# Performance work log

Measured on AMD Instinct MI355X. Metric: run time of the kernel, lower is better.

## Reference

```python
import jax, jax.numpy as jnp
import numpy as np

B, N, C_IN, C_EMB, G = 16, 1024, 16, 64, 128
NEG = -1e12


def _lap(m):
    # m @ D^-1/2, transpose, @ D^-1/2  (matches torch code incl. transpose)
    d = jnp.sum(m, axis=1) ** -0.5
    return (m * d[None, :]).T * d[None, :]


def setup_inputs():
    key = jax.random.key(0)
    ks = jax.random.split(key, 16)
    f = jax.random.normal
    return {
        'x': f(ks[0], (B, C_IN, N), jnp.float32),
        'ct': f(ks[1], (B, C_EMB, N), jnp.float32),
        'graph_data': jax.random.uniform(ks[2], (2, N, N), dtype=jnp.float32),
        'emb_w': f(ks[3], (C_EMB, C_IN)) / np.sqrt(C_IN).astype(np.float32),
        'emb_b': f(ks[4], (C_EMB,)) * 0.01,
        'emb2_w': f(ks[5], (N, N)) / np.sqrt(N).astype(np.float32),
        'emb2_b': f(ks[6], (N,)) * 0.01,
        'att_W': f(ks[7], (C_EMB, C_EMB)) / np.sqrt(C_EMB).astype(np.float32),
        'att_a': f(ks[8], (2 * C_EMB, 1)) / np.sqrt(2 * C_EMB).astype(np.float32),
        'att_GL': f(ks[9], (N, G)) / np.sqrt(G).astype(np.float32),
        'uai_w': f(ks[10], (C_EMB, C_EMB)) / np.sqrt(C_EMB).astype(np.float32),
        'uai_b': f(ks[11], (C_EMB,)) * 0.01,
        'lin1_w': f(ks[12], (C_EMB, C_EMB)) / np.sqrt(C_EMB).astype(np.float32),
        'lin2_w': f(ks[13], (C_EMB, C_EMB)) / np.sqrt(C_EMB).astype(np.float32),
        'lin2_b': f(ks[14], (C_EMB,)) * 0.01,
        'ln_w': jnp.ones((C_EMB, N), jnp.float32),
        'ln_b': jnp.zeros((C_EMB, N), jnp.float32),
    }


def reference(x, ct, graph_data, emb_w, emb_b, emb2_w, emb2_b, att_W, att_a,
              att_GL, uai_w, uai_b, lin1_w, lin2_w, lin2_b, ln_w, ln_b):
    # emb: Conv1d k=1 -> leaky_relu -> Linear over node axis N
    h0 = jax.nn.leaky_relu(jnp.einsum('bcn,ec->ben', x, emb_w) + emb_b[None, :, None])
    h0 = jnp.einsum('ben,mn->bem', h0, emb2_w) + emb2_b[None, None, :]
    inp = jnp.swapaxes(h0, 1, 2)  # [B,N,C']

    # InterpositionAttention (repeat/cat factorized: e_ij = leakyrelu(a1.h_i + a2.h_j))
    eye = jnp.eye(N, dtype=x.dtype)
    adj_att = jax.nn.softmax(jax.nn.relu(att_GL @ att_GL.T), axis=-1) + eye
    h = inp @ att_W  # [B,N,C']
    e = jax.nn.leaky_relu((h @ att_a[:C_EMB]) + jnp.swapaxes(h @ att_a[C_EMB:], 1, 2))  # [B,N,N]
    att = jax.nn.softmax(jnp.where(adj_att > 0, e, NEG), axis=2)
    x_att = jnp.swapaxes(jax.nn.relu(att @ h), 1, 2)  # [B,C',N]

    # UAI module (eval mode: dropout off -> all MC samples equal -> sigma = 0)
    mu = jnp.swapaxes(x_att, 1, 2) @ uai_w.T + uai_b  # [B,N,C']
    x_uai = jnp.swapaxes(mu, 1, 2)  # [B,C',N]

    g1 = _lap(graph_data[0] + eye)
    g2 = _lap(graph_data[1] + eye)

    # learned adjacency from pairwise squared distances (cdist p=2, squared)
    xf = jnp.swapaxes(x_uai, 1, 2)  # [B,N,C']
    sq = jnp.sum(xf * xf, axis=-1)
    d2 = jnp.maximum(sq[:, :, None] + sq[:, None, :] - 2.0 * (xf @ jnp.swapaxes(xf, 1, 2)), 0.0)
    gl = jax.nn.softmax(jnp.exp(-d2 / (2.0 * C_EMB)) + eye, axis=-1)  # sigma^2 = emb_size

    def ln(z):  # LayerNorm over last two dims [C', N]
        m = jnp.mean(z, axis=(1, 2), keepdims=True)
        v = jnp.var(z, axis=(1, 2), keepdims=True)
        return (z - m) / jnp.sqrt(v + 1e-5) * ln_w + ln_b

    l1 = lambda z: jnp.einsum('oc,bcn->bon', lin1_w, z)
    l2 = lambda z: jnp.einsum('oc,bcn->bon', lin2_w, z) + lin2_b[None, :, None]

    x_new = ln(l1(x_uai) @ gl + l1(l1(x_uai) @ g1) @ g2)
    ft = jax.nn.gelu(ln(l2(x_uai) @ gl + l2(l2(x_uai) @ g1) @ g2), approximate=False)
    rt = ft  # rt is computed by the identical expression (dropout off)

    ct_new = ft * ct + x_new - ft * x_new
    ht = rt * jax.nn.elu(ct_new) + x_uai - rt * x_uai
    return (ht, ct_new)
```

## Files before the change

kernel.cpp:

```cpp
#include <hip/hip_runtime.h>
#include <math.h>

typedef unsigned short u16;
typedef __attribute__((ext_vector_type(8))) short short8;
typedef __attribute__((ext_vector_type(4))) float floatx4;

constexpr int BATCH = 16;
constexpr int NI = 1024;
constexpr int CE = 64;
constexpr int CI = 16;
constexpr long long NN2  = (long long)NI * NI;
constexpr long long BCN  = (long long)BATCH * CE * NI;
constexpr long long BNv  = (long long)BATCH * NI;
constexpr long long BNN  = (long long)BATCH * NI * NI;
constexpr long long S1 = (long long)CE * NI;
constexpr long long S2 = 2 * S1;
constexpr int ZERON = (int)(2 * BNv + 80);

__device__ __forceinline__ float lrelu01(float x) { return x > 0.f ? x : 0.01f * x; }

__device__ __forceinline__ u16 f2bf(float f) {
  unsigned u = __builtin_bit_cast(unsigned, f);
  return (u16)((u + 0x7fffu + ((u >> 16) & 1u)) >> 16);
}
__device__ __forceinline__ float bf2f(u16 h) {
  unsigned u = ((unsigned)h) << 16;
  return __builtin_bit_cast(float, u);
}
__device__ __forceinline__ unsigned fkey(float f) {
  unsigned u = __builtin_bit_cast(unsigned, f);
  return (u & 0x80000000u) ? ~u : (u | 0x80000000u);
}
__device__ __forceinline__ float funkey(unsigned k) {
  unsigned u = (k & 0x80000000u) ? (k & 0x7fffffffu) : ~k;
  return __builtin_bit_cast(float, u);
}

__device__ __forceinline__ void gload16(const u16* g, u16* l) {
  __builtin_amdgcn_global_load_lds(
      (const __attribute__((address_space(1))) void*)g,
      (__attribute__((address_space(3))) void*)l, 16, 0, 0);
}

__device__ __forceinline__ void fence13() {
  __builtin_amdgcn_sched_barrier(0);
  asm volatile("s_waitcnt vmcnt(2) lgkmcnt(0)" ::: "memory");
  __builtin_amdgcn_s_barrier();
  __builtin_amdgcn_sched_barrier(0);
}

template<int N>
__device__ __forceinline__ void fence_bar() {
  __builtin_amdgcn_sched_barrier(0);
  if constexpr (N == 0) asm volatile("s_waitcnt vmcnt(0)" ::: "memory");
  else if constexpr (N == 1) asm volatile("s_waitcnt vmcnt(1)" ::: "memory");
  else if constexpr (N == 2) asm volatile("s_waitcnt vmcnt(2)" ::: "memory");
  else if constexpr (N == 3) asm volatile("s_waitcnt vmcnt(3)" ::: "memory");
  else if constexpr (N == 4) asm volatile("s_waitcnt vmcnt(4)" ::: "memory");
  else if constexpr (N == 6) asm volatile("s_waitcnt vmcnt(6)" ::: "memory");
  else if constexpr (N == 8) asm volatile("s_waitcnt vmcnt(8)" ::: "memory");
  else asm volatile("s_waitcnt vmcnt(0)" ::: "memory");
  __builtin_amdgcn_s_barrier();
  __builtin_amdgcn_sched_barrier(0);
}

template<int BM, int BN, int MODE>
__global__ __launch_bounds__(256) void mgemm(
    const u16* __restrict__ Ag, const u16* __restrict__ B1g, const u16* __restrict__ B2g,
    int K1, int K, int lda, int ldb, long long bsA, long long bsB1,
    float* __restrict__ Cf, u16* __restrict__ Cb, int ldc, long long bsC,
    const float* __restrict__ aux1, const float* __restrict__ aux2,
    const float* __restrict__ aux3, const float* __restrict__ aux4,
    float* __restrict__ Zout)
{
  constexpr int RM = BM / 2, RN = BN / 2, MI = RM / 16, NJ = RN / 16;
  constexpr bool PIPE3 = (MODE == 5 || MODE == 14 || MODE == 15);
  constexpr int DEPTH = 3;
  constexpr int NBB = PIPE3 ? DEPTH : (MODE == 13 ? 3 : 1);
  constexpr int NBA = PIPE3 ? DEPTH : (MODE == 13 ? 2 : 1);
  constexpr int NLA = (BM * 8) / 256;
  constexpr int NLB = (BN * 8) / 256;
  constexpr int L = (MODE == 13) ? NLB : (NLA + NLB);
  __shared__ __align__(16) u16 As[NBA * BM * 64];
  __shared__ __align__(16) u16 Bs[NBB * BN * 64];
  __shared__ __align__(16) u16 xa[MODE == 13 ? 32 * 72 : 1];
  const int tid = threadIdx.x;
  int z, n0, r0, job15 = 0;
  bool job4 = false;
  long long cboff = 0;
  if constexpr (MODE == 15) {
    const int id = blockIdx.x;
    if (id >= 512 && id < 1536) {
      const int m = id - 512;
      float s = 0.f, sv = 0.f;
      for (int n = tid; n < NI; n += 256) {
        float g = aux3[(long long)m * NI + n] * aux2[n];
        s += g;
        sv = fmaf(g, aux1[n], sv);
      }
      float* r1 = (float*)As;
      float* r2 = (float*)As + 256;
      r1[tid] = s; r2[tid] = sv; __syncthreads();
      for (int st = 128; st > 0; st >>= 1) {
        if (tid < st) { r1[tid] += r1[tid + st]; r2[tid] += r2[tid + st]; }
        __syncthreads();
      }
      if (tid == 0) {
        float dm = aux2[m];
        Cf[m] = dm * (r1[0] + dm);
        Zout[m] = dm * (r2[0] + dm * aux1[m]);
      }
      return;
    }
    if (id >= 1536) {
      const int id2 = id - 1536;
      job15 = 2;
      z = id2 >> 5; r0 = (id2 & 1) * BM; n0 = ((id2 >> 1) & 15) * BN;
    } else {
      z = 0; n0 = (id & 15) * BN; r0 = (id >> 4) * BM;
    }
  } else if constexpr (MODE == 5) {
    const int fid = blockIdx.x;
    const int xcd = fid & 7, idx = fid >> 3;
    const int code = (idx >> 5) * 8 + xcd;
    z = code >> 1; r0 = (code & 1) * BM; n0 = (idx & 31) * BN;
  } else if constexpr (MODE == 3) {
    const int id = blockIdx.x;
    if (id < 4096) {
      const int xcd = id & 7, idx = id >> 3;
      z = (idx >> 8) * 8 + xcd;
      const int g = idx & 255;
      n0 = (g & 15) * 64; r0 = ((g >> 4) & 15) * 64;
    } else {
      const int t = id - 4096;
      job4 = true;
      z = t >> 5;
      const int yblk = 2 + ((t >> 4) & 1);
      r0 = yblk * 64;
      n0 = (t & 15) * 64;
    }
  } else if constexpr (MODE == 13 || MODE == 14) {
    const int id = blockIdx.x;
    const int xcd = id & 7, idx = id >> 3;
    z = (idx >> 5) * 8 + xcd;
    if constexpr (MODE == 13) { r0 = (idx & 31) * BM; n0 = 0; }
    else { n0 = (idx & 31) * BN; r0 = 0; }
  } else {
    z = blockIdx.z; n0 = blockIdx.x * BN; r0 = blockIdx.y * BM;
  }
  int Kv = K, K1v = K1, ldav = lda, ldbv = ldb;
  const u16 *Ab, *Bb1;
  if constexpr (MODE == 15) {
    if (job15 == 2) {
      Kv = 64; K1v = 128; ldav = 64; ldbv = 64;
      Ab = B2g + (long long)r0 * 64;
      Bb1 = (const u16*)aux4 + (long long)z * S1 + (long long)n0 * 64;
      cboff = bsB1 + (long long)z * S1;
    } else {
      Ab = Ag + (long long)r0 * lda;
      Bb1 = B1g + (long long)n0 * ldb;
    }
  } else {
    Ab = Ag + (long long)z * bsA + (long long)r0 * ldav;
    Bb1 = B1g + (long long)z * bsB1 + (long long)n0 * ldbv;
    if constexpr (MODE == 3) {
      if (job4) Ab = ((const u16*)aux2) + (long long)r0 * 64;
    }
  }
  const int lane = tid & 63;
  const int wid = tid >> 6;
  const int wr = wid >> 1, wc = wid & 1;
  const int q = lane >> 4, mlow = lane & 15;
  const int wbase = tid & ~63;

  floatx4 acc[MI][NJ] = {};
  float zp0 = 0.f;

  float s1r_13 = 0.f, mr_13 = 0.f;
  const float* s2z_13 = nullptr;
  float4 sa, sb;
  if constexpr (MODE == 13) {
    const float* s1z = aux2 + (long long)z * NI;
    s2z_13 = aux3 + (long long)z * NI;
    const float mb = funkey(((const unsigned*)aux4)[z]);
    s1r_13 = s1z[r0 + (tid >> 3)];
    mr_13 = lrelu01(s1r_13 + mb);
  }

  auto stageAB = [&](int buf, int k0) {
    if constexpr (MODE != 13) {
      const u16* Asrc = Ab + k0;
#pragma unroll
      for (int s = 0; s < NLA; s++) {
        int cid = tid + s * 256;
        int r = cid >> 3, cc = cid & 7;
        gload16(Asrc + (long long)r * ldav + ((cc ^ (r & 7)) << 3),
                As + buf * (BM * 64) + ((wbase + s * 256) << 3));
      }
    }
    const u16* Bsrc = (k0 < K1v) ? (Bb1 + k0)
                                 : (B2g + (long long)n0 * ldbv + (k0 - K1v));
#pragma unroll
    for (int s = 0; s < NLB; s++) {
      int cid = tid + s * 256;
      int r = cid >> 3, cc = cid & 7;
      gload16(Bsrc + (long long)r * ldbv + ((cc ^ (r & 7)) << 3),
              Bs + buf * (BN * 64) + ((wbase + s * 256) << 3));
    }
  };

  auto agen_ld = [&](int k0) {
    const float* sp = s2z_13 + k0 + (tid & 7) * 8;
    sa = *(const float4*)sp;
    sb = *(const float4*)(sp + 4);
  };
  auto agen_st = [&](int buf) {
    int r = tid >> 3, craw = tid & 7;
    float p0 = __expf(lrelu01(s1r_13 + sa.x) - mr_13);
    float p1 = __expf(lrelu01(s1r_13 + sa.y) - mr_13);
    float p2 = __expf(lrelu01(s1r_13 + sa.z) - mr_13);
    float p3 = __expf(lrelu01(s1r_13 + sa.w) - mr_13);
    float p4 = __expf(lrelu01(s1r_13 + sb.x) - mr_13);
    float p5 = __expf(lrelu01(s1r_13 + sb.y) - mr_13);
    float p6 = __expf(lrelu01(s1r_13 + sb.z) - mr_13);
    float p7 = __expf(lrelu01(s1r_13 + sb.w) - mr_13);
    zp0 += p0 + p1 + p2 + p3 + p4 + p5 + p6 + p7;
    uint4 v;
    v.x = (unsigned)f2bf(p0) | ((unsigned)f2bf(p1) << 16);
    v.y = (unsigned)f2bf(p2) | ((unsigned)f2bf(p3) << 16);
    v.z = (unsigned)f2bf(p4) | ((unsigned)f2bf(p5) << 16);
    v.w = (unsigned)f2bf(p6) | ((unsigned)f2bf(p7) << 16);
    *(uint4*)&As[buf * (BM * 64) + (r * 8 + (craw ^ (r & 7))) * 8] = v;
  };

  auto compute_tile = [&](int bufA, int bufB) {
#pragma unroll
    for (int kh = 0; kh < 2; kh++) {
      const int kc = kh * 4 + q;
      short8 afr[MI], bfr[NJ];
#pragma unroll
      for (int i = 0; i < MI; i++) {
        int row = wr * RM + i * 16 + mlow;
        afr[i] = *(const short8*)&As[bufA * (BM * 64) + (row * 8 + (kc ^ (row & 7))) * 8];
      }
#pragma unroll
      for (int j = 0; j < NJ; j++) {
        int row = wc * RN + j * 16 + mlow;
        bfr[j] = *(const short8*)&Bs[bufB * (BN * 64) + (row * 8 + (kc ^ (row & 7))) * 8];
      }
#pragma unroll
      for (int i = 0; i < MI; i++)
#pragma unroll
        for (int j = 0; j < NJ; j++)
          acc[i][j] = __builtin_amdgcn_mfma_f32_16x16x32_bf16(afr[i], bfr[j], acc[i][j], 0, 0, 0);
    }
  };

  if constexpr (PIPE3) {
    const int nk = Kv >> 6;
#pragma unroll
    for (int p = 0; p < DEPTH - 1; p++) {
      int kk = (p < nk) ? p : (nk - 1);
      stageAB(p, kk << 6);
    }
    fence_bar<(DEPTH - 2) * L>();
    int cur = 0, stg = DEPTH - 1;
    for (int ki = 0; ki < nk; ki++) {
      if (ki + DEPTH - 1 < nk) stageAB(stg, (ki + DEPTH - 1) << 6);
      compute_tile(cur, cur);
      if (ki + 1 < nk) {
        const int rem = nk - 1 - ki;
        const int u = (rem < DEPTH - 1) ? rem : (DEPTH - 1);
        if (u == 2) fence_bar<L>();
        else fence_bar<0>();
      }
      cur++; if (cur == NBB) cur = 0;
      stg++; if (stg == NBB) stg = 0;
    }
    __syncthreads();
  } else if constexpr (MODE == 13) {
    const int nk = Kv >> 6;
    agen_ld(0);
    stageAB(0, 0);
    if (nk > 1) stageAB(1, 64);
    agen_st(0);
    fence13();
    for (int ki = 0; ki < nk; ki++) {
      if (ki + 1 < nk) agen_ld((ki + 1) << 6);
      if (ki + 2 < nk) stageAB((ki + 2) % 3, (ki + 2) << 6);
      if (ki + 1 < nk) agen_st((ki + 1) & 1);
      compute_tile(ki & 1, ki % 3);
      fence13();
    }
  } else {
    for (int k0 = 0; k0 < Kv; k0 += 64) {
      stageAB(0, k0);
      __syncthreads();
      compute_tile(0, 0);
      __syncthreads();
    }
  }

  if constexpr (MODE == 3) {
    if (job4) {
      u16* abig = (u16*)Cf;
#pragma unroll
      for (int i = 0; i < MI; i++) {
#pragma unroll
        for (int j = 0; j < NJ; j++) {
#pragma unroll
          for (int rg = 0; rg < 4; rg++) {
            int r = r0 + wr * RM + i * 16 + q * 4 + rg;
            int ncol = n0 + wc * RN + j * 16 + mlow;
            int blk = r >> 6, oo = r & 63;
            int drow = ((blk & 1) << 6) + oo;
            abig[(long long)z * (128 * 2048LL) + (long long)drow * 2048 + 1024 + ncol] =
                f2bf(acc[i][j][rg]);
          }
        }
      }
    } else {
      const float* sqb = aux1 + (long long)z * NI;
#pragma unroll
      for (int i = 0; i < MI; i++) {
#pragma unroll
        for (int rg = 0; rg < 4; rg++) {
          int r = r0 + wr * RM + i * 16 + q * 4 + rg;
          float sqi = sqb[r];
          float rsum = 0.f;
#pragma unroll
          for (int j = 0; j < NJ; j++) {
            int ncol = n0 + wc * RN + j * 16 + mlow;
            float d2 = fmaxf(sqi + sqb[ncol] - 2.f * acc[i][j][rg], 0.f);
            float w = __expf(__expf(-d2 * (1.f / 128.f)) + (r == ncol ? 1.f : 0.f) - 2.f);
            Cb[(long long)z * bsC + (long long)r * ldc + ncol] = f2bf(w);
            rsum += w;
          }
          rsum += __shfl_xor(rsum, 1);
          rsum += __shfl_xor(rsum, 2);
          rsum += __shfl_xor(rsum, 4);
          rsum += __shfl_xor(rsum, 8);
          if (mlow == 0) atomicAdd(&Zout[(long long)z * NI + r], rsum);
        }
      }
    }
  } else if constexpr (MODE == 14) {
    float ps1 = 0.f, ps2 = 0.f;
#pragma unroll
    for (int i = 0; i < MI; i++) {
#pragma unroll
      for (int rg = 0; rg < 4; rg++) {
        int r = wr * RM + i * 16 + q * 4 + rg;
        int ncol = n0 + wc * RN + mlow;
        float v = acc[i][0][rg] + aux3[r] * aux1[ncol];
        Cb[(long long)z * bsC + (long long)r * ldc + ncol] = f2bf(v);
        ps1 = fmaf(v, aux2[r], ps1);
        ps2 = fmaf(v, aux2[64 + r], ps2);
      }
    }
    ps1 += __shfl_xor(ps1, 16); ps1 += __shfl_xor(ps1, 32);
    ps2 += __shfl_xor(ps2, 16); ps2 += __shfl_xor(ps2, 32);
    float* sred = (float*)As;
    const int col = wc * RN + mlow;
    if (q == 0) { sred[col * 2 + wr] = ps1; sred[64 + col * 2 + wr] = ps2; }
    __syncthreads();
    if (tid < 32) {
      float v1 = sred[tid * 2] + sred[tid * 2 + 1];
      float v2 = sred[64 + tid * 2] + sred[64 + tid * 2 + 1];
      Cf[(long long)z * NI + n0 + tid] = v1;
      Zout[(long long)z * NI + n0 + tid] = v2;
      float mx = v2;
      for (int off = 1; off < 32; off <<= 1) mx = fmaxf(mx, __shfl_xor(mx, off));
      if (tid == 0) atomicMax((unsigned*)B2g + z, fkey(mx));
    }
  } else if constexpr (MODE == 13) {
    float* zred = (float*)xa;
    float* zinv = (float*)xa + 256;
    zred[(tid >> 3) * 8 + (tid & 7)] = zp0;
    __syncthreads();
    if (tid < 32) {
      float sum = 0.f;
#pragma unroll
      for (int j = 0; j < 8; j++) sum += zred[tid * 8 + j];
      zinv[tid] = 1.f / sum;
    }
    __syncthreads();
    float zr[4];
#pragma unroll
    for (int rg = 0; rg < 4; rg++) zr[rg] = zinv[wr * 16 + q * 4 + rg];
    __syncthreads();
#pragma unroll
    for (int j = 0; j < NJ; j++) {
#pragma unroll
      for (int rg = 0; rg < 4; rg++) {
        int row = wr * 16 + q * 4 + rg;
        int col = wc * RN + j * 16 + mlow;
        float v = fmaxf(acc[0][j][rg] * zr[rg], 0.f);
        xa[row * 72 + col] = f2bf(v);
      }
    }
#pragma unroll
    for (int s = 0; s < 2; s++) {
      int cid = tid + s * 256;
      int r = cid >> 3, cc = cid & 7;
      gload16(B2g + r * 64 + ((cc ^ (r & 7)) << 3),
              Bs + ((wbase + s * 256) << 3));
    }
    __syncthreads();
    floatx4 acc2[2] = {};
#pragma unroll
    for (int kh = 0; kh < 2; kh++) {
      const int kc = kh * 4 + q;
      short8 a2 = *(const short8*)&xa[(wr * 16 + mlow) * 72 + kc * 8];
#pragma unroll
      for (int j = 0; j < 2; j++) {
        int orow = wc * 32 + j * 16 + mlow;
        short8 b2 = *(const short8*)&Bs[(orow * 8 + (kc ^ (orow & 7))) * 8];
        acc2[j] = __builtin_amdgcn_mfma_f32_16x16x32_bf16(a2, b2, acc2[j], 0, 0, 0);
      }
    }
#pragma unroll
    for (int rg = 0; rg < 4; rg++) {
      int row = r0 + wr * 16 + q * 4 + rg;
      float sqp = 0.f;
#pragma unroll
      for (int j = 0; j < 2; j++) {
        int o = wc * 32 + j * 16 + mlow;
        float v = acc2[j][rg] + aux1[o];
        Cb[(long long)z * bsC + (long long)row * ldc + o] = f2bf(v);
        sqp = fmaf(v, v, sqp);
      }
      sqp += __shfl_xor(sqp, 1);
      sqp += __shfl_xor(sqp, 2);
      sqp += __shfl_xor(sqp, 4);
      sqp += __shfl_xor(sqp, 8);
      if (mlow == 0) atomicAdd(&Zout[(long long)z * NI + row], sqp);
    }
  } else if constexpr (MODE == 5) {
    float ts = 0.f, tss = 0.f;
#pragma unroll
    for (int i = 0; i < MI; i++) {
#pragma unroll
      for (int j = 0; j < NJ; j++) {
#pragma unroll
        for (int rg = 0; rg < 4; rg++) {
          int r = r0 + wr * RM + i * 16 + q * 4 + rg;
          int ncol = n0 + wc * RN + j * 16 + mlow;
          float v = acc[i][j][rg];
          v += aux3[r] * aux1[ncol] + aux4[r] * aux2[ncol];
          Cb[(long long)z * bsC + (long long)r * ldc + ncol] = f2bf(v);
          ts += v;
          tss = fmaf(v, v, tss);
        }
      }
    }
    float* red = (float*)As;
    red[tid] = ts; red[256 + tid] = tss;
    __syncthreads();
    for (int st = 128; st > 0; st >>= 1) {
      if (tid < st) { red[tid] += red[tid + st]; red[256 + tid] += red[256 + tid + st]; }
      __syncthreads();
    }
    if (tid == 0) {
      const int half = r0 >> 6;
      atomicAdd(&Zout[z * 2 + half], red[0]);
      atomicAdd(&Zout[32 + z * 2 + half], red[256]);
    }
  } else {
#pragma unroll
    for (int i = 0; i < MI; i++) {
#pragma unroll
      for (int j = 0; j < NJ; j++) {
#pragma unroll
        for (int rg = 0; rg < 4; rg++) {
          int r = r0 + wr * RM + i * 16 + q * 4 + rg;
          int ncol = n0 + wc * RN + j * 16 + mlow;
          float v = acc[i][j][rg];
          if constexpr (MODE == 4) {
            int blk = r >> 6, oo = r & 63;
            int drow = ((blk & 1) << 6) + oo;
            if (blk < 2) v = (v + aux3[drow]) / aux1[(long long)z * NI + ncol];
            Cb[(long long)z * bsC + (long long)drow * 2048 + (long long)(blk >> 1) * 1024 + ncol] =
                f2bf(v);
          } else if constexpr (MODE == 15) {
            Cb[cboff + (long long)r * ldc + ncol] = f2bf(v);
          } else {
            Cb[(long long)z * bsC + (long long)r * ldc + ncol] = f2bf(v);
          }
        }
      }
    }
  }
}

__global__ __launch_bounds__(256) void lap_rowsum(const float* __restrict__ gd,
                                                  float* __restrict__ dr,
                                                  float* __restrict__ zero)
{
  if (blockIdx.x >= 2048) {
    int i = (blockIdx.x - 2048) * 256 + threadIdx.x;
    if (i < ZERON) zero[i] = 0.f;
    return;
  }
  const int ki = blockIdx.x;
  const float* row = gd + (long long)ki * NI;
  float s = 0.f;
  for (int j = threadIdx.x; j < NI; j += 256) s += row[j];
  __shared__ float red[256];
  red[threadIdx.x] = s; __syncthreads();
  for (int st = 128; st > 0; st >>= 1) {
    if (threadIdx.x < st) red[threadIdx.x] += red[threadIdx.x + st];
    __syncthreads();
  }
  if (threadIdx.x == 0) dr[ki] = rsqrtf(red[0] + 1.f);
}

__global__ __launch_bounds__(256) void mega_prep(
    const float* __restrict__ l1w, const float* __restrict__ l2w,
    const float* __restrict__ l2b, const float* __restrict__ uaiw,
    const float* __restrict__ attW,
    u16* __restrict__ stack4, float* __restrict__ rb2ext, float* __restrict__ rl2ext,
    u16* __restrict__ uaiw_bf, u16* __restrict__ attwT_bf, float* __restrict__ wcs,
    const float* __restrict__ emb2w, u16* __restrict__ emb2w_bf,
    const float* __restrict__ x, const float* __restrict__ ew,
    const float* __restrict__ eb, u16* __restrict__ h0aT,
    const float* __restrict__ gd, const float* __restrict__ dsum,
    u16* __restrict__ g2t, u16* __restrict__ g1,
    float* __restrict__ cs1)
{
  __shared__ float sm[1092];
  const int bid = blockIdx.x;
  const int t = threadIdx.x;
  if (bid < 98) {
    const int gid = bid * 256 + t;
    if (gid < 4096) {
      stack4[gid] = f2bf(l1w[gid]);
    } else if (gid < 8192) {
      stack4[gid] = f2bf(l2w[gid - 4096]);
    } else if (gid < 12288) {
      int tt = gid - 8192, o = tt >> 6, m = tt & 63;
      float s = 0.f;
      for (int c = 0; c < 64; c++) s = fmaf(l1w[o * 64 + c], l1w[c * 64 + m], s);
      stack4[gid] = f2bf(s);
    } else if (gid < 16384) {
      int tt = gid - 12288, o = tt >> 6, m = tt & 63;
      float s = 0.f;
      for (int c = 0; c < 64; c++) s = fmaf(l2w[o * 64 + c], l2w[c * 64 + m], s);
      stack4[gid] = f2bf(s);
    } else if (gid < 16512) {
      int r = gid - 16384;
      rb2ext[r] = (r < 64) ? 0.f : l2b[r - 64];
    } else if (gid < 16640) {
      int r = gid - 16512;
      float v = 0.f;
      if (r >= 64) { int o = r - 64; for (int c = 0; c < 64; c++) v = fmaf(l2w[o * 64 + c], l2b[c], v); }
      rl2ext[r] = v;
    } else if (gid < 20736) {
      uaiw_bf[gid - 16640] = f2bf(uaiw[gid - 16640]);
    } else if (gid < 24832) {
      int idx = gid - 20736;
      int c = idx >> 6, e = idx & 63;
      attwT_bf[idx] = f2bf(attW[e * 64 + c]);
    } else if (gid < 24896) {
      int c = gid - 24832;
      float s = 0.f;
      for (int e = 0; e < 64; e++) s += attW[e * 64 + c];
      wcs[c] = s;
    }
  } else if (bid < 4194) {
    const long long i = (long long)(bid - 98) * 256 + t;
    emb2w_bf[i] = f2bf(emb2w[i]);
  } else if (bid < 4450) {
    const int sub = bid - 4194;
    const int b = sub >> 4;
    const int nc = (sub & 15) * 64;
    float* we = sm;
    float* be = sm + 1024;
    for (int i = t; i < 1024; i += 256) we[i] = ew[i];
    if (t < 64) be[t] = eb[t];
    __syncthreads();
    const int n = nc + (t >> 2);
    const int e0 = (t & 3) * 16;
    const float* xb = x + (long long)b * CI * NI + n;
    float xv[16];
#pragma unroll
    for (int c = 0; c < CI; c++) xv[c] = xb[(long long)c * NI];
    u16 out16[16];
#pragma unroll
    for (int ee = 0; ee < 16; ee++) {
      const int e = e0 + ee;
      float a = be[e];
#pragma unroll
      for (int c = 0; c < CI; c++) a = fmaf(xv[c], we[e * 16 + c], a);
      out16[ee] = f2bf(lrelu01(a));
    }
    u16* dst = h0aT + (long long)b * S1 + (long long)n * 64 + e0;
    *(uint4*)dst = *(uint4*)out16;
    *(uint4*)(dst + 8) = *(uint4*)(out16 + 8);
  } else if (bid < 8546) {
    const long long idx = (long long)(bid - 4450) * 256 + t;
    const int m = (int)(idx >> 10), j = (int)(idx & 1023);
    const float* d = dsum + NI;
    float v = (gd[NN2 + idx] + (m == j ? 1.f : 0.f)) * d[m] * d[j];
    g2t[idx] = f2bf(v);
  } else if (bid < 9570) {
    const int sub = bid - 8546;
    const int bx = (sub & 31) * 32, by = (sub >> 5) * 32;
    const int lx = t & 31, ly = t >> 5;
    float* tile = sm;
    for (int yy = ly; yy < 32; yy += 8)
      tile[yy * 33 + lx] = gd[(long long)(by + yy) * NI + bx + lx];
    __syncthreads();
    for (int yy = ly; yy < 32; yy += 8) {
      const int i = bx + yy, j = by + lx;
      float v = (tile[lx * 33 + yy] + (i == j ? 1.f : 0.f)) * dsum[i] * dsum[j];
      g1[(long long)i * NI + j] = f2bf(v);
    }
  } else {
    const int n = bid - 9570;
    float s = 0.f;
    for (int i = t; i < NI; i += 256) s = fmaf(gd[(long long)n * NI + i], dsum[i], s);
    float* red = sm;
    red[t] = s; __syncthreads();
    for (int st = 128; st > 0; st >>= 1) {
      if (t < st) red[t] += red[t + st];
      __syncthreads();
    }
    if (t == 0) cs1[n] = dsum[n] * (red[0] + dsum[n]);
  }
}

__global__ __launch_bounds__(512) void ln_final_t(const u16* __restrict__ T,
                                                  const float* __restrict__ stats,
                                                  const float* __restrict__ lnw,
                                                  const float* __restrict__ lnb,
                                                  const float* __restrict__ ct,
                                                  const u16* __restrict__ xuT,
                                                  float* __restrict__ outp)
{
  __shared__ float xs[64 * 65];
  const int blk = blockIdx.x;
  const int b = blk >> 4;
  const int n0 = (blk & 15) << 6;
  const int t = threadIdx.x;
  const int tc = t & 63, tr = t >> 6;
#pragma unroll
  for (int i = 0; i < 8; i++) {
    int nn = i * 8 + tr;
    xs[tc * 65 + nn] = bf2f(xuT[((long long)b << 16) + (long long)(n0 + nn) * 64 + tc]);
  }
  __syncthreads();
  const float inv_n = 1.f / 65536.f;
  const float m0 = stats[b * 2] * inv_n;
  const float m1 = stats[b * 2 + 1] * inv_n;
  const float rs0 = rsqrtf(fmaxf(stats[32 + b * 2] * inv_n - m0 * m0, 0.f) + 1e-5f);
  const float rs1 = rsqrtf(fmaxf(stats[32 + b * 2 + 1] * inv_n - m1 * m1, 0.f) + 1e-5f);
#pragma unroll
  for (int j = 0; j < 8; j++) {
    const int c = j * 8 + tr;
    const int n = n0 + tc;
    const int rem = c * NI + n;
    const long long toff = (long long)b * S2 + rem;
    const float t0 = bf2f(T[toff]);
    const float t1 = bf2f(T[toff + S1]);
    const float w = lnw[rem], bb = lnb[rem];
    const float xn = (t0 - m0) * rs0 * w + bb;
    float ft = (t1 - m1) * rs1 * w + bb;
    ft = 0.5f * ft * (1.f + erff(ft * 0.70710678118654752f));
    const float u = xs[c * 65 + tc];
    const long long oidx = ((long long)b << 16) + rem;
    const float cn = fmaf(ft, ct[oidx] - xn, xn);
    const float el = cn > 0.f ? cn : expm1f(cn);
    outp[oidx] = fmaf(ft, el - u, u);
    outp[BCN + oidx] = cn;
  }
}

extern "C" void kernel_launch(void* const* d_in, const int* in_sizes, int n_in,
                              void* d_out, int out_size, void* d_ws, size_t ws_size,
                              hipStream_t stream)
{
  (void)in_sizes; (void)n_in; (void)out_size; (void)ws_size;
  const float* x      = (const float*)d_in[0];
  const float* ct     = (const float*)d_in[1];
  const float* gdata  = (const float*)d_in[2];
  const float* emb_w  = (const float*)d_in[3];
  const float* emb_b  = (const float*)d_in[4];
  const float* emb2_w = (const float*)d_in[5];
  const float* emb2_b = (const float*)d_in[6];
  const float* att_W  = (const float*)d_in[7];
  const float* att_a  = (const float*)d_in[8];
  const float* uai_w  = (const float*)d_in[10];
  const float* uai_b  = (const float*)d_in[11];
  const float* lin1_w = (const float*)d_in[12];
  const float* lin2_w = (const float*)d_in[13];
  const float* lin2_b = (const float*)d_in[14];
  const float* ln_w   = (const float*)d_in[15];
  const float* ln_b   = (const float*)d_in[16];
  float* outp = (float*)d_out;

  float* ws = (float*)d_ws;
  long long o = 0;
  auto af = [&](long long n) { float* p = ws + o; o += (n + 63) & ~63LL; return p; };
  auto au = [&](long long n) { return (u16*)af((n + 1) / 2); };

  float* s1      = af(BNv);
  float* s2      = af(BNv);
  float* dsum    = af(2 * NI);
  float* cs1v    = af(NI);
  float* cs2v    = af(NI);
  float* v2v     = af(NI);
  float* rb2ext  = af(128);
  float* rl2ext  = af(128);
  float* wcs     = af(64);
  float* zeroreg = af(ZERON);
  float* Zgl     = zeroreg;
  float* sqv     = zeroreg + BNv;
  float* stats   = zeroreg + 2 * BNv;
  unsigned* s2mU = (unsigned*)(stats + 64);
  u16* Tacc      = au(S2 * BATCH);
  u16* emb2w_bf  = au(NN2);
  u16* h0aTb     = au(S1 * BATCH);
  u16* ybf       = au(S1 * BATCH);
  u16* hTb       = au(S1 * BATCH);
  u16* xuaiTb    = au(S1 * BATCH);
  u16* g1b       = au(NN2);
  u16* g2tb      = au(NN2);
  u16* G12b      = au(NN2);
  u16* Abig      = au((long long)BATCH * 128 * 2048);
  u16* stack4    = au(256 * 64);
  u16* uaiw_bf   = au(CE * CE);
  u16* attwT_bf  = au(CE * CE);
  u16* bigW      = au(BNN);

  lap_rowsum<<<2048 + (ZERON + 255) / 256, 256, 0, stream>>>(gdata, dsum, zeroreg);

  mega_prep<<<10594, 256, 0, stream>>>(
      lin1_w, lin2_w, lin2_b, uai_w, att_W,
      stack4, rb2ext, rl2ext, uaiw_bf, attwT_bf, wcs,
      emb2_w, emb2w_bf, x, emb_w, emb_b, h0aTb,
      gdata, dsum, g2tb, g1b, cs1v);

  mgemm<32, 64, 15><<<2048, 256, 0, stream>>>(
      g2tb, g1b, attwT_bf, NI, NI, NI, NI, 0, (long long)(ybf - G12b),
      cs2v, G12b, NI, 0, cs1v, dsum + NI, gdata + NN2, (const float*)h0aTb, v2v);

  mgemm<64, 32, 14><<<512, 256, 0, stream>>>(
      ybf, emb2w_bf, (const u16*)s2mU, NI, NI, NI, NI, S1, 0,
      s1, hTb, NI, S1, emb2_b, att_a, wcs, nullptr, s2);

  mgemm<32, 64, 13><<<512, 256, 0, stream>>>(
      hTb, hTb, uaiw_bf, NI, NI, NI, NI, 0, S1,
      nullptr, xuaiTb, CE, S1, uai_b, s1, s2, (const float*)s2mU, sqv);

  mgemm<64, 64, 3><<<4608, 256, 0, stream>>>(
      xuaiTb, xuaiTb, nullptr, CE, CE, CE, CE, S1, S1,
      (float*)Abig, bigW, NI, NN2, sqv, (const float*)stack4, nullptr, nullptr, Zgl);

  mgemm<64, 64, 4><<<dim3(16, 2, BATCH), 256, 0, stream>>>(
      stack4, xuaiTb, nullptr, CE, CE, CE, CE, 0, S1,
      nullptr, Abig, 0, (long long)128 * 2048, Zgl, nullptr, rb2ext, nullptr, nullptr);

  mgemm<64, 32, 5><<<1024, 256, 0, stream>>>(
      Abig, bigW, G12b, NI, 2 * NI, 2048, NI, (long long)128 * 2048, NN2,
      nullptr, Tacc, NI, S2, cs2v, v2v, rb2ext, rl2ext, stats);

  ln_final_t<<<256, 512, 0, stream>>>(Tacc, stats, ln_w, ln_b, ct, xuaiTb, outp);
}
```

Measured before the change: 225.8 us.

## Split final GEMM K dimension in two with fp32 atomic accumulation and separate LN stats

```diff
diff --git a/kernel.cpp b/kernel.cpp
--- a/kernel.cpp
+++ b/kernel.cpp
@@ -16,6 +16,8 @@
 constexpr long long S1 = (long long)CE * NI;
 constexpr long long S2 = 2 * S1;
 constexpr int ZERON = (int)(2 * BNv + 80);
+constexpr long long ZPAD = ((long long)ZERON + 63) & ~63LL;
+constexpr long long ZTOT = ZPAD + S2 * BATCH;
 
 __device__ __forceinline__ float lrelu01(float x) { return x > 0.f ? x : 0.01f * x; }
 
@@ -85,7 +87,7 @@
   __shared__ __align__(16) u16 Bs[NBB * BN * 64];
   __shared__ __align__(16) u16 xa[MODE == 13 ? 32 * 72 : 1];
   const int tid = threadIdx.x;
-  int z, n0, r0, job15 = 0;
+  int z, n0, r0, job15 = 0, chunk5 = 0;
   bool job4 = false;
   long long cboff = 0;
   if constexpr (MODE == 15) {
@@ -122,8 +124,10 @@
   } else if constexpr (MODE == 5) {
     const int fid = blockIdx.x;
     const int xcd = fid & 7, idx = fid >> 3;
-    const int code = (idx >> 5) * 8 + xcd;
-    z = code >> 1; r0 = (code & 1) * BM; n0 = (idx & 31) * BN;
+    const int code32 = (idx >> 6) * 8 + xcd;
+    z = code32 >> 1; chunk5 = code32 & 1;
+    const int sub = idx & 63;
+    r0 = (sub >> 5) * BM; n0 = (sub & 31) * BN;
   } else if constexpr (MODE == 3) {
     const int id = blockIdx.x;
     if (id < 4096) {
@@ -165,6 +169,10 @@
     Bb1 = B1g + (long long)z * bsB1 + (long long)n0 * ldbv;
     if constexpr (MODE == 3) {
       if (job4) Ab = ((const u16*)aux2) + (long long)r0 * 64;
+    }
+    if constexpr (MODE == 5) {
+      Ab += chunk5 << 10;
+      if (chunk5) Bb1 = B2g + (long long)n0 * ldbv;
     }
   }
   const int lane = tid & 63;
@@ -437,7 +445,6 @@
       if (mlow == 0) atomicAdd(&Zout[(long long)z * NI + row], sqp);
     }
   } else if constexpr (MODE == 5) {
-    float ts = 0.f, tss = 0.f;
 #pragma unroll
     for (int i = 0; i < MI; i++) {
 #pragma unroll
@@ -446,25 +453,9 @@
         for (int rg = 0; rg < 4; rg++) {
           int r = r0 + wr * RM + i * 16 + q * 4 + rg;
           int ncol = n0 + wc * RN + j * 16 + mlow;
-          float v = acc[i][j][rg];
-          v += aux3[r] * aux1[ncol] + aux4[r] * aux2[ncol];
-          Cb[(long long)z * bsC + (long long)r * ldc + ncol] = f2bf(v);
-          ts += v;
-          tss = fmaf(v, v, tss);
+          atomicAdd(&Cf[(long long)z * bsC + (long long)r * ldc + ncol], acc[i][j][rg]);
         }
       }
-    }
-    float* red = (float*)As;
-    red[tid] = ts; red[256 + tid] = tss;
-    __syncthreads();
-    for (int st = 128; st > 0; st >>= 1) {
-      if (tid < st) { red[tid] += red[tid + st]; red[256 + tid] += red[256 + tid + st]; }
-      __syncthreads();
-    }
-    if (tid == 0) {
-      const int half = r0 >> 6;
-      atomicAdd(&Zout[z * 2 + half], red[0]);
-      atomicAdd(&Zout[32 + z * 2 + half], red[256]);
     }
   } else {
 #pragma unroll
@@ -498,8 +489,11 @@
                                                   float* __restrict__ zero)
 {
   if (blockIdx.x >= 2048) {
-    int i = (blockIdx.x - 2048) * 256 + threadIdx.x;
-    if (i < ZERON) zero[i] = 0.f;
+    long long i = (long long)(blockIdx.x - 2048) * 1024 + (long long)threadIdx.x * 4;
+    if (i < ZTOT) {
+      float4 zz = {0.f, 0.f, 0.f, 0.f};
+      *(float4*)(zero + i) = zz;
+    }
     return;
   }
   const int ki = blockIdx.x;
@@ -630,12 +624,54 @@
   }
 }
 
-__global__ __launch_bounds__(512) void ln_final_t(const u16* __restrict__ T,
+__global__ __launch_bounds__(256) void ln_stats(
+    const float* __restrict__ T, const float* __restrict__ rb2,
+    const float* __restrict__ rl2, const float* __restrict__ cs2,
+    const float* __restrict__ v2, float* __restrict__ stats)
+{
+  const int bid = blockIdx.x;
+  const int b = bid >> 5;
+  const int rbase = (bid & 31) * 4;
+  const int t = threadIdx.x;
+  const float4 c4 = ((const float4*)cs2)[t];
+  const float4 w4 = ((const float4*)v2)[t];
+  float ts = 0.f, tss = 0.f;
+#pragma unroll
+  for (int rr = 0; rr < 4; rr++) {
+    const int r = rbase + rr;
+    const float a3 = rb2[r], a4 = rl2[r];
+    float4 t4 = ((const float4*)(T + (long long)b * S2 + (long long)r * NI))[t];
+    float v0 = t4.x + a3 * c4.x + a4 * w4.x;
+    float v1 = t4.y + a3 * c4.y + a4 * w4.y;
+    float v2e = t4.z + a3 * c4.z + a4 * w4.z;
+    float v3 = t4.w + a3 * c4.w + a4 * w4.w;
+    ts += v0 + v1 + v2e + v3;
+    tss = fmaf(v0, v0, fmaf(v1, v1, fmaf(v2e, v2e, fmaf(v3, v3, tss))));
+  }
+  __shared__ float red[512];
+  red[t] = ts; red[256 + t] = tss;
+  __syncthreads();
+  for (int st = 128; st > 0; st >>= 1) {
+    if (t < st) { red[t] += red[t + st]; red[256 + t] += red[256 + t + st]; }
+    __syncthreads();
+  }
+  if (t == 0) {
+    const int half = rbase >> 6;
+    atomicAdd(&stats[b * 2 + half], red[0]);
+    atomicAdd(&stats[32 + b * 2 + half], red[256]);
+  }
+}
+
+__global__ __launch_bounds__(512) void ln_final_t(const float* __restrict__ Tf,
                                                   const float* __restrict__ stats,
                                                   const float* __restrict__ lnw,
                                                   const float* __restrict__ lnb,
                                                   const float* __restrict__ ct,
                                                   const u16* __restrict__ xuT,
+                                                  const float* __restrict__ cs2,
+                                                  const float* __restrict__ v2x,
+                                                  const float* __restrict__ rb2,
+                                                  const float* __restrict__ rl2,
                                                   float* __restrict__ outp)
 {
   __shared__ float xs[64 * 65];
@@ -661,8 +697,8 @@
     const int n = n0 + tc;
     const int rem = c * NI + n;
     const long long toff = (long long)b * S2 + rem;
-    const float t0 = bf2f(T[toff]);
-    const float t1 = bf2f(T[toff + S1]);
+    const float t0 = Tf[toff];
+    const float t1 = Tf[toff + S1] + rb2[64 + c] * cs2[n] + rl2[64 + c] * v2x[n];
     const float w = lnw[rem], bb = lnb[rem];
     const float xn = (t0 - m0) * rs0 * w + bb;
     float ft = (t1 - m1) * rs1 * w + bb;
@@ -718,7 +754,7 @@
   float* sqv     = zeroreg + BNv;
   float* stats   = zeroreg + 2 * BNv;
   unsigned* s2mU = (unsigned*)(stats + 64);
-  u16* Tacc      = au(S2 * BATCH);
+  float* TaccF   = af(S2 * BATCH);
   u16* emb2w_bf  = au(NN2);
   u16* h0aTb     = au(S1 * BATCH);
   u16* ybf       = au(S1 * BATCH);
@@ -733,7 +769,8 @@
   u16* attwT_bf  = au(CE * CE);
   u16* bigW      = au(BNN);
 
-  lap_rowsum<<<2048 + (ZERON + 255) / 256, 256, 0, stream>>>(gdata, dsum, zeroreg);
+  lap_rowsum<<<2048 + (int)((ZTOT + 1023) / 1024), 256, 0, stream>>>(
+      gdata, dsum, zeroreg);
 
   mega_prep<<<10594, 256, 0, stream>>>(
       lin1_w, lin2_w, lin2_b, uai_w, att_W,
@@ -761,9 +798,12 @@
       stack4, xuaiTb, nullptr, CE, CE, CE, CE, 0, S1,
       nullptr, Abig, 0, (long long)128 * 2048, Zgl, nullptr, rb2ext, nullptr, nullptr);
 
-  mgemm<64, 32, 5><<<1024, 256, 0, stream>>>(
-      Abig, bigW, G12b, NI, 2 * NI, 2048, NI, (long long)128 * 2048, NN2,
-      nullptr, Tacc, NI, S2, cs2v, v2v, rb2ext, rl2ext, stats);
-
-  ln_final_t<<<256, 512, 0, stream>>>(Tacc, stats, ln_w, ln_b, ct, xuaiTb, outp);
-}
+  mgemm<64, 32, 5><<<2048, 256, 0, stream>>>(
+      Abig, bigW, G12b, NI, NI, 2048, NI, (long long)128 * 2048, NN2,
+      TaccF, nullptr, NI, S2, nullptr, nullptr, nullptr, nullptr, nullptr);
+
+  ln_stats<<<512, 256, 0, stream>>>(TaccF, rb2ext, rl2ext, cs2v, v2v, stats);
+
+  ln_final_t<<<256, 512, 0, stream>>>(TaccF, stats, ln_w, ln_b, ct, xuaiTb,
+                                      cs2v, v2v, rb2ext, rl2ext, outp);
+}
```

Result: slower. 236.2 us (+4.6%).

## Fold mode-4 GEMM into mode-3 launch and apply softmax normalizer in mode-5 B load

Applied to the files above, without the earlier changes.

```diff
diff --git a/kernel.cpp b/kernel.cpp
--- a/kernel.cpp
+++ b/kernel.cpp
@@ -49,6 +49,13 @@
   __builtin_amdgcn_sched_barrier(0);
 }
 
+__device__ __forceinline__ void fence5() {
+  __builtin_amdgcn_sched_barrier(0);
+  asm volatile("s_waitcnt vmcnt(2) lgkmcnt(0)" ::: "memory");
+  __builtin_amdgcn_s_barrier();
+  __builtin_amdgcn_sched_barrier(0);
+}
+
 template<int N>
 __device__ __forceinline__ void fence_bar() {
   __builtin_amdgcn_sched_barrier(0);
@@ -58,7 +65,6 @@
   else if constexpr (N == 3) asm volatile("s_waitcnt vmcnt(3)" ::: "memory");
   else if constexpr (N == 4) asm volatile("s_waitcnt vmcnt(4)" ::: "memory");
   else if constexpr (N == 6) asm volatile("s_waitcnt vmcnt(6)" ::: "memory");
-  else if constexpr (N == 8) asm volatile("s_waitcnt vmcnt(8)" ::: "memory");
   else asm volatile("s_waitcnt vmcnt(0)" ::: "memory");
   __builtin_amdgcn_s_barrier();
   __builtin_amdgcn_sched_barrier(0);
@@ -74,13 +80,12 @@
     float* __restrict__ Zout)
 {
   constexpr int RM = BM / 2, RN = BN / 2, MI = RM / 16, NJ = RN / 16;
-  constexpr bool PIPE3 = (MODE == 5 || MODE == 14 || MODE == 15);
-  constexpr int DEPTH = 3;
-  constexpr int NBB = PIPE3 ? DEPTH : (MODE == 13 ? 3 : 1);
-  constexpr int NBA = PIPE3 ? DEPTH : (MODE == 13 ? 2 : 1);
+  constexpr bool PIPE3 = (MODE == 14 || MODE == 15);
+  constexpr int NBB = PIPE3 ? 3 : (MODE == 13 ? 3 : (MODE == 5 ? 2 : 1));
+  constexpr int NBA = PIPE3 ? 3 : (MODE == 13 ? 2 : (MODE == 5 ? 3 : 1));
   constexpr int NLA = (BM * 8) / 256;
   constexpr int NLB = (BN * 8) / 256;
-  constexpr int L = (MODE == 13) ? NLB : (NLA + NLB);
+  constexpr int L = (NLA + NLB);
   __shared__ __align__(16) u16 As[NBA * BM * 64];
   __shared__ __align__(16) u16 Bs[NBB * BN * 64];
   __shared__ __align__(16) u16 xa[MODE == 13 ? 32 * 72 : 1];
@@ -132,12 +137,12 @@
       const int g = idx & 255;
       n0 = (g & 15) * 64; r0 = ((g >> 4) & 15) * 64;
     } else {
-      const int t = id - 4096;
+      const int t4 = id - 4096;
       job4 = true;
-      z = t >> 5;
-      const int yblk = 2 + ((t >> 4) & 1);
-      r0 = yblk * 64;
-      n0 = (t & 15) * 64;
+      z = t4 >> 6;
+      const int g = t4 & 63;
+      r0 = (g >> 4) * 64;
+      n0 = (g & 15) * 64;
     }
   } else if constexpr (MODE == 13 || MODE == 14) {
     const int id = blockIdx.x;
@@ -259,23 +264,76 @@
   if constexpr (PIPE3) {
     const int nk = Kv >> 6;
 #pragma unroll
-    for (int p = 0; p < DEPTH - 1; p++) {
+    for (int p = 0; p < 2; p++) {
       int kk = (p < nk) ? p : (nk - 1);
       stageAB(p, kk << 6);
     }
-    fence_bar<(DEPTH - 2) * L>();
-    int cur = 0, stg = DEPTH - 1;
+    fence_bar<L>();
+    int cur = 0, stg = 2;
     for (int ki = 0; ki < nk; ki++) {
-      if (ki + DEPTH - 1 < nk) stageAB(stg, (ki + DEPTH - 1) << 6);
+      if (ki + 2 < nk) stageAB(stg, (ki + 2) << 6);
       compute_tile(cur, cur);
       if (ki + 1 < nk) {
         const int rem = nk - 1 - ki;
-        const int u = (rem < DEPTH - 1) ? rem : (DEPTH - 1);
+        const int u = (rem < 2) ? rem : 2;
         if (u == 2) fence_bar<L>();
         else fence_bar<0>();
       }
       cur++; if (cur == NBB) cur = 0;
       stg++; if (stg == NBB) stg = 0;
+    }
+    __syncthreads();
+  } else if constexpr (MODE == 5) {
+    const int nk = Kv >> 6;
+    const float* Zg = Cf + (long long)z * NI;
+    uint4 bv; float4 bz0, bz1;
+    const int br = tid >> 3, bcc = tid & 7;
+    auto aglo = [&](int kt, int buf) {
+      const u16* Asrc = Ab + (kt << 6);
+#pragma unroll
+      for (int s = 0; s < NLA; s++) {
+        int cid = tid + s * 256;
+        int r = cid >> 3, cc = cid & 7;
+        gload16(Asrc + (long long)r * ldav + ((cc ^ (r & 7)) << 3),
+                As + buf * (BM * 64) + ((wbase + s * 256) << 3));
+      }
+    };
+    auto bld = [&](int kt) {
+      const int k0 = kt << 6;
+      const u16* Bsrc = (k0 < K1v) ? (Bb1 + k0)
+                                   : (B2g + (long long)n0 * ldbv + (k0 - K1v));
+      bv = *(const uint4*)(Bsrc + (long long)br * ldbv + bcc * 8);
+      if (k0 < K1v) {
+        bz0 = *(const float4*)(Zg + k0 + bcc * 8);
+        bz1 = *(const float4*)(Zg + k0 + bcc * 8 + 4);
+      }
+    };
+    auto bst = [&](int kt, int buf) {
+      uint4 w = bv;
+      if ((kt << 6) < K1v) {
+        float f0 = bf2f((u16)(w.x & 0xffff)) * __builtin_amdgcn_rcpf(bz0.x);
+        float f1 = bf2f((u16)(w.x >> 16))    * __builtin_amdgcn_rcpf(bz0.y);
+        float f2 = bf2f((u16)(w.y & 0xffff)) * __builtin_amdgcn_rcpf(bz0.z);
+        float f3 = bf2f((u16)(w.y >> 16))    * __builtin_amdgcn_rcpf(bz0.w);
+        float f4 = bf2f((u16)(w.z & 0xffff)) * __builtin_amdgcn_rcpf(bz1.x);
+        float f5 = bf2f((u16)(w.z >> 16))    * __builtin_amdgcn_rcpf(bz1.y);
+        float f6 = bf2f((u16)(w.w & 0xffff)) * __builtin_amdgcn_rcpf(bz1.z);
+        float f7 = bf2f((u16)(w.w >> 16))    * __builtin_amdgcn_rcpf(bz1.w);
+        w.x = (unsigned)f2bf(f0) | ((unsigned)f2bf(f1) << 16);
+        w.y = (unsigned)f2bf(f2) | ((unsigned)f2bf(f3) << 16);
+        w.z = (unsigned)f2bf(f4) | ((unsigned)f2bf(f5) << 16);
+        w.w = (unsigned)f2bf(f6) | ((unsigned)f2bf(f7) << 16);
+      }
+      *(uint4*)&Bs[buf * (BN * 64) + (br * 8 + (bcc ^ (br & 7))) * 8] = w;
+    };
+    bld(0); aglo(0, 0); aglo(1, 1); bst(0, 0);
+    fence5();
+    for (int ki = 0; ki < nk; ki++) {
+      if (ki + 1 < nk) bld(ki + 1);
+      if (ki + 2 < nk) aglo(ki + 2, (ki + 2) % 3);
+      if (ki + 1 < nk) bst(ki + 1, (ki + 1) & 1);
+      compute_tile(ki % 3, ki & 1);
+      fence5();
     }
     __syncthreads();
   } else if constexpr (MODE == 13) {
@@ -314,8 +372,10 @@
             int ncol = n0 + wc * RN + j * 16 + mlow;
             int blk = r >> 6, oo = r & 63;
             int drow = ((blk & 1) << 6) + oo;
-            abig[(long long)z * (128 * 2048LL) + (long long)drow * 2048 + 1024 + ncol] =
-                f2bf(acc[i][j][rg]);
+            float v = acc[i][j][rg];
+            if (blk < 2) v += aux3[drow];
+            abig[(long long)z * (128 * 2048LL) + (long long)drow * 2048 +
+                 (long long)(blk >> 1) * 1024 + ncol] = f2bf(v);
           }
         }
       }
@@ -475,18 +535,7 @@
         for (int rg = 0; rg < 4; rg++) {
           int r = r0 + wr * RM + i * 16 + q * 4 + rg;
           int ncol = n0 + wc * RN + j * 16 + mlow;
-          float v = acc[i][j][rg];
-          if constexpr (MODE == 4) {
-            int blk = r >> 6, oo = r & 63;
-            int drow = ((blk & 1) << 6) + oo;
-            if (blk < 2) v = (v + aux3[drow]) / aux1[(long long)z * NI + ncol];
-            Cb[(long long)z * bsC + (long long)drow * 2048 + (long long)(blk >> 1) * 1024 + ncol] =
-                f2bf(v);
-          } else if constexpr (MODE == 15) {
-            Cb[cboff + (long long)r * ldc + ncol] = f2bf(v);
-          } else {
-            Cb[(long long)z * bsC + (long long)r * ldc + ncol] = f2bf(v);
-          }
+          Cb[cboff + (long long)r * ldc + ncol] = f2bf(acc[i][j][rg]);
         }
       }
     }
@@ -567,11 +616,13 @@
       for (int e = 0; e < 64; e++) s += attW[e * 64 + c];
       wcs[c] = s;
     }
-  } else if (bid < 4194) {
-    const long long i = (long long)(bid - 98) * 256 + t;
-    emb2w_bf[i] = f2bf(emb2w[i]);
-  } else if (bid < 4450) {
-    const int sub = bid - 4194;
+  } else if (bid < 1122) {
+    const long long i = (long long)(bid - 98) * 1024 + t * 4;
+    float4 v = *(const float4*)(emb2w + i);
+    u16 o4[4] = {f2bf(v.x), f2bf(v.y), f2bf(v.z), f2bf(v.w)};
+    *(uint2*)(emb2w_bf + i) = *(const uint2*)o4;
+  } else if (bid < 1378) {
+    const int sub = bid - 1122;
     const int b = sub >> 4;
     const int nc = (sub & 15) * 64;
     float* we = sm;
@@ -597,14 +648,21 @@
     u16* dst = h0aT + (long long)b * S1 + (long long)n * 64 + e0;
     *(uint4*)dst = *(uint4*)out16;
     *(uint4*)(dst + 8) = *(uint4*)(out16 + 8);
-  } else if (bid < 8546) {
-    const long long idx = (long long)(bid - 4450) * 256 + t;
-    const int m = (int)(idx >> 10), j = (int)(idx & 1023);
+  } else if (bid < 2402) {
+    const int m = bid - 1378;
+    const int j = t * 4;
     const float* d = dsum + NI;
-    float v = (gd[NN2 + idx] + (m == j ? 1.f : 0.f)) * d[m] * d[j];
-    g2t[idx] = f2bf(v);
-  } else if (bid < 9570) {
-    const int sub = bid - 8546;
+    float4 g = *(const float4*)(gd + NN2 + (long long)m * NI + j);
+    float dm = d[m];
+    float4 dj = *(const float4*)(d + j);
+    u16 o4[4];
+    o4[0] = f2bf((g.x + (m == j     ? 1.f : 0.f)) * dm * dj.x);
+    o4[1] = f2bf((g.y + (m == j + 1 ? 1.f : 0.f)) * dm * dj.y);
+    o4[2] = f2bf((g.z + (m == j + 2 ? 1.f : 0.f)) * dm * dj.z);
+    o4[3] = f2bf((g.w + (m == j + 3 ? 1.f : 0.f)) * dm * dj.w);
+    *(uint2*)(g2t + (long long)m * NI + j) = *(const uint2*)o4;
+  } else if (bid < 3426) {
+    const int sub = bid - 2402;
     const int bx = (sub & 31) * 32, by = (sub >> 5) * 32;
     const int lx = t & 31, ly = t >> 5;
     float* tile = sm;
@@ -617,7 +675,7 @@
       g1[(long long)i * NI + j] = f2bf(v);
     }
   } else {
-    const int n = bid - 9570;
+    const int n = bid - 3426;
     float s = 0.f;
     for (int i = t; i < NI; i += 256) s = fmaf(gd[(long long)n * NI + i], dsum[i], s);
     float* red = sm;
@@ -735,7 +793,7 @@
 
   lap_rowsum<<<2048 + (ZERON + 255) / 256, 256, 0, stream>>>(gdata, dsum, zeroreg);
 
-  mega_prep<<<10594, 256, 0, stream>>>(
+  mega_prep<<<4450, 256, 0, stream>>>(
       lin1_w, lin2_w, lin2_b, uai_w, att_W,
       stack4, rb2ext, rl2ext, uaiw_bf, attwT_bf, wcs,
       emb2_w, emb2w_bf, x, emb_w, emb_b, h0aTb,
@@ -753,17 +811,13 @@
       hTb, hTb, uaiw_bf, NI, NI, NI, NI, 0, S1,
       nullptr, xuaiTb, CE, S1, uai_b, s1, s2, (const float*)s2mU, sqv);
 
-  mgemm<64, 64, 3><<<4608, 256, 0, stream>>>(
+  mgemm<64, 64, 3><<<5120, 256, 0, stream>>>(
       xuaiTb, xuaiTb, nullptr, CE, CE, CE, CE, S1, S1,
-      (float*)Abig, bigW, NI, NN2, sqv, (const float*)stack4, nullptr, nullptr, Zgl);
-
-  mgemm<64, 64, 4><<<dim3(16, 2, BATCH), 256, 0, stream>>>(
-      stack4, xuaiTb, nullptr, CE, CE, CE, CE, 0, S1,
-      nullptr, Abig, 0, (long long)128 * 2048, Zgl, nullptr, rb2ext, nullptr, nullptr);
+      (float*)Abig, bigW, NI, NN2, sqv, (const float*)stack4, rb2ext, nullptr, Zgl);
 
   mgemm<64, 32, 5><<<1024, 256, 0, stream>>>(
       Abig, bigW, G12b, NI, 2 * NI, 2048, NI, (long long)128 * 2048, NN2,
-      nullptr, Tacc, NI, S2, cs2v, v2v, rb2ext, rl2ext, stats);
+      Zgl, Tacc, NI, S2, cs2v, v2v, rb2ext, rl2ext, stats);
 
   ln_final_t<<<256, 512, 0, stream>>>(Tacc, stats, ln_w, ln_b, ct, xuaiTb, outp);
 }
```

Result: no change. 222.7 us (-1.4%).
